# Performance work log

Hardware: AMD Instinct MI355X
Metric: run time of the kernel (lower is better)

Reference implementation:

```python
import jax, jax.numpy as jnp
import numpy as np

B, S, H, NH, HD = 2, 2048, 1024, 16, 64
RD = 16            # rotary_dim = head_dim * 0.25
W = 16             # mini_context_length (sliding window)
SCALE = HD ** -0.5
ROPE_BASE = 10000.0


def setup_inputs() -> dict:
    key = jax.random.key(0)
    ks = jax.random.split(key, 10)
    p = lambda k, shape: (jax.random.normal(k, shape, dtype=jnp.float32) * 0.02)
    return {
        "hidden_states": jax.random.normal(ks[0], (B, S, H), dtype=jnp.float32),
        "Wqkv": p(ks[1], (3 * H, H)), "bqkv": p(ks[2], (3 * H,)),
        "Wqa": p(ks[3], (H, H)),      "bqa": p(ks[4], (H,)),
        "Wka": p(ks[5], (H, H)),      "bka": p(ks[6], (H,)),
        "Wd": p(ks[7], (H, H)),       "bd": p(ks[8], (H,)),
    }


def _rotate_half(x):
    x1, x2 = jnp.split(x, 2, axis=-1)
    return jnp.concatenate([-x2, x1], axis=-1)


def _apply_rope(q, k, seq_len):
    # GPT-NeoX style rotary on the first RD dims. q,k: [B,NH,S,RD]
    inv_freq = 1.0 / (ROPE_BASE ** (jnp.arange(0, RD, 2, dtype=jnp.float32) / RD))
    t = jnp.arange(seq_len, dtype=jnp.float32)
    freqs = jnp.outer(t, inv_freq)                     # [S, RD//2]
    emb = jnp.concatenate([freqs, freqs], axis=-1)     # [S, RD]
    cos = jnp.cos(emb)[None, None]                      # [1,1,S,RD]
    sin = jnp.sin(emb)[None, None]
    return q * cos + _rotate_half(q) * sin, k * cos + _rotate_half(k) * sin


def reference(hidden_states, Wqkv, bqkv, Wqa, bqa, Wka, bka, Wd, bd):
    b, s, _ = hidden_states.shape
    qkv = hidden_states @ Wqkv.T + bqkv                       # [B,S,3H]
    qkv = qkv.reshape(b, s, 3, NH, HD).transpose(2, 0, 3, 1, 4)
    q, k, v = qkv[0], qkv[1], qkv[2]                          # [B,NH,S,HD]

    q_rot, k_rot = _apply_rope(q[..., :RD], k[..., :RD], s)
    q = jnp.concatenate([q_rot, q[..., RD:]], axis=-1)
    k = jnp.concatenate([k_rot, k[..., RD:]], axis=-1)

    # ----- Stage 1: sliding-window local attention (vectorized) -----
    pos = jnp.arange(s)
    idx = pos[:, None] - (W - 1) + jnp.arange(W)[None, :]     # [S,W]
    valid = idx >= 0
    idxc = jnp.clip(idx, 0, s - 1)
    k_win = k[:, :, idxc, :]                                   # [B,NH,S,W,HD]
    v_win = v[:, :, idxc, :]
    scores = jnp.einsum('bhsd,bhswd->bhsw', q, k_win) * SCALE
    scores = jnp.where(valid[None, None], scores, -jnp.inf)
    probs = jax.nn.softmax(scores, axis=-1)
    A = jnp.einsum('bhsw,bhswd->bhsd', probs, v_win)           # [B,NH,S,HD]

    A_hidden = A.transpose(0, 2, 1, 3).reshape(b, s, H)        # [B,S,H]

    # ----- Stage 2: causal global attention over A -----
    qa = (A_hidden @ Wqa.T + bqa).reshape(b, s, NH, HD).transpose(0, 2, 1, 3)
    ka = (A_hidden @ Wka.T + bka).reshape(b, s, NH, HD).transpose(0, 2, 1, 3)
    g = jnp.einsum('bhqd,bhkd->bhqk', qa, ka) * SCALE          # [B,NH,S,S]
    causal = pos[:, None] >= pos[None, :]
    g = jnp.where(causal[None, None], g, -jnp.inf)
    pg = jax.nn.softmax(g, axis=-1)
    out = jnp.einsum('bhqk,bhkd->bhqd', pg, A)                 # [B,NH,S,HD]
    out = out.transpose(0, 2, 1, 3).reshape(b, s, H)
    return out @ Wd.T + bd
```

## Files before the change

### kernel.cpp

```cpp
#include <hip/hip_runtime.h>
#include <hip/hip_bf16.h>
#include <cstdint>
#include <cstddef>

typedef __bf16 bf16;
typedef __bf16 bf16x4 __attribute__((ext_vector_type(4)));
typedef __bf16 bf16x8 __attribute__((ext_vector_type(8)));
typedef float  f32x4  __attribute__((ext_vector_type(4)));

#define DEVINL __device__ __forceinline__

constexpr int   Bc  = 2, Sc = 2048, Hc = 1024, NHc = 16, HDc = 64;
constexpr int   Tc  = Bc * Sc;
constexpr float L2E = 1.44269504088896340736f;
constexpr float NEG_BIG = -1.0e30f;
constexpr float INV2PI = 0.15915494309189535f;

typedef __attribute__((address_space(1))) void AS1void;
typedef __attribute__((address_space(3))) void AS3void;

DEVINL void load_lds16(const bf16* g, bf16* l) {
  __builtin_amdgcn_global_load_lds((AS1void*)g, (AS3void*)l, 16, 0, 0);
}

#if __has_builtin(__builtin_amdgcn_exp2f)
DEVINL float fast_exp2(float x) { return __builtin_amdgcn_exp2f(x); }
#else
DEVINL float fast_exp2(float x) { return exp2f(x); }
#endif

#if __has_builtin(__builtin_amdgcn_sinf) && __has_builtin(__builtin_amdgcn_cosf) && __has_builtin(__builtin_amdgcn_fractf)
DEVINL void fast_sincos_rev(float rev, float* sn, float* cs) {
  float r = __builtin_amdgcn_fractf(rev);
  *sn = __builtin_amdgcn_sinf(r);
  *cs = __builtin_amdgcn_cosf(r);
}
#else
DEVINL void fast_sincos_rev(float rev, float* sn, float* cs) {
  sincosf(rev * 6.283185307179586f, sn, cs);
}
#endif

DEVINL void xcd_remap(int& mi, int& ni) {
  const int nx  = (int)gridDim.x;
  const int nwg = nx * (int)gridDim.y;
  const int flat = (int)blockIdx.y * nx + (int)blockIdx.x;
  const int nper = nwg >> 3;
  const int neu  = (flat & 7) * nper + (flat >> 3);
  mi = neu / nx; ni = neu - mi * nx;
}

__global__ __launch_bounds__(256)
void convert_all(const float* __restrict__ hs, const float* __restrict__ Wqkv,
                 const float* __restrict__ Wqa, const float* __restrict__ Wka,
                 const float* __restrict__ Wd, const float* __restrict__ bqa,
                 const float* __restrict__ bka,
                 bf16* __restrict__ hsb, bf16* __restrict__ wqkvb,
                 bf16* __restrict__ wqakab, bf16* __restrict__ wdb,
                 float* __restrict__ bqaka) {
  const int blk = blockIdx.x;
  if (blk >= 5120) {
    const int i = threadIdx.x * 8;
    const float* src = (i < 1024) ? (bqa + i) : (bka + i - 1024);
    *(f32x4*)(bqaka + i)     = *(const f32x4*)src;
    *(f32x4*)(bqaka + i + 4) = *(const f32x4*)(src + 4);
    return;
  }
  const float* src; bf16* dst; int base;
  if      (blk < 2048) { src = hs;   dst = hsb;                    base = blk; }
  else if (blk < 3584) { src = Wqkv; dst = wqkvb;                  base = blk - 2048; }
  else if (blk < 4096) { src = Wqa;  dst = wqakab;                 base = blk - 3584; }
  else if (blk < 4608) { src = Wka;  dst = wqakab + 1024 * 1024;   base = blk - 4096; }
  else                 { src = Wd;   dst = wdb;                    base = blk - 4608; }
  const int i = (base * 256 + threadIdx.x) * 8;
  f32x4 a = *(const f32x4*)(src + i);
  f32x4 b = *(const f32x4*)(src + i + 4);
  bf16x8 v;
#pragma unroll
  for (int j = 0; j < 4; j++) { v[j] = (bf16)a[j]; v[4 + j] = (bf16)b[j]; }
  *(bf16x8*)(dst + i) = v;
}

template <typename CT>
__global__ __launch_bounds__(256, 3)
void gemm128(const bf16* __restrict__ A, const bf16* __restrict__ Bw,
             const float* __restrict__ bias, CT* __restrict__ C,
             int M, int N, int K) {
  __shared__ __attribute__((aligned(16))) bf16 As[128 * 64];
  __shared__ __attribute__((aligned(16))) bf16 Bs[128 * 64];

  const int tid = threadIdx.x, wv = tid >> 6, lane = tid & 63;
  int mi, ni; xcd_remap(mi, ni);
  const int m0 = mi * 128, n0 = ni * 128;
  const int col = lane & 15, quad = lane >> 4;
  const int wrow = (wv >> 1) * 64, wcol = (wv & 1) * 64;

  f32x4 acc[4][4];
#pragma unroll
  for (int i = 0; i < 4; i++)
#pragma unroll
    for (int j = 0; j < 4; j++) acc[i][j] = f32x4{0.f, 0.f, 0.f, 0.f};

  const int srow = tid >> 3;
  const int scol = (((tid & 7) ^ (srow & 7)) << 3);
  const bf16* Ag = A  + (size_t)(m0 + srow) * K + scol;
  const bf16* Bg = Bw + (size_t)(n0 + srow) * K + scol;
  const int cs = col & 7;

  for (int k0 = 0; k0 < K; k0 += 64) {
#pragma unroll
    for (int c = 0; c < 4; c++) {
      load_lds16(Ag + (size_t)(c * 32) * K + k0, As + c * 2048 + tid * 8);
      load_lds16(Bg + (size_t)(c * 32) * K + k0, Bs + c * 2048 + tid * 8);
    }
    __syncthreads();
#pragma unroll
    for (int kk = 0; kk < 64; kk += 32) {
      const int so = ((((kk >> 3) + quad) ^ cs) << 3);
      bf16x8 af[4], bfr[4];
#pragma unroll
      for (int i = 0; i < 4; i++)
        af[i] = *(const bf16x8*)(As + (wrow + i * 16 + col) * 64 + so);
#pragma unroll
      for (int j = 0; j < 4; j++)
        bfr[j] = *(const bf16x8*)(Bs + (wcol + j * 16 + col) * 64 + so);
#pragma unroll
      for (int i = 0; i < 4; i++)
#pragma unroll
        for (int j = 0; j < 4; j++)
          acc[i][j] = __builtin_amdgcn_mfma_f32_16x16x32_bf16(af[i], bfr[j], acc[i][j], 0, 0, 0);
    }
    __syncthreads();
  }

#pragma unroll
  for (int j = 0; j < 4; j++) {
    const int c = n0 + wcol + j * 16 + col;
    const float bv = bias[c];
#pragma unroll
    for (int i = 0; i < 4; i++)
#pragma unroll
      for (int r = 0; r < 4; r++) {
        const int rr = m0 + wrow + i * 16 + quad * 4 + r;
        C[(size_t)rr * N + c] = (CT)(acc[i][j][r] + bv);
      }
  }
}

template <typename CT>
__global__ __launch_bounds__(256, 3)
void gemm12864(const bf16* __restrict__ A, const bf16* __restrict__ Bw,
               const float* __restrict__ bias, CT* __restrict__ C,
               int M, int N, int K) {
  __shared__ __attribute__((aligned(16))) bf16 As[128 * 64];
  __shared__ __attribute__((aligned(16))) bf16 Bs[64 * 64];

  const int tid = threadIdx.x, wv = tid >> 6, lane = tid & 63;
  int mi, ni; xcd_remap(mi, ni);
  const int m0 = mi * 128, n0 = ni * 64;
  const int col = lane & 15, quad = lane >> 4;
  const int wm = wv >> 1, wn = wv & 1;

  f32x4 acc[4][2];
#pragma unroll
  for (int i = 0; i < 4; i++)
#pragma unroll
    for (int j = 0; j < 2; j++) acc[i][j] = f32x4{0.f, 0.f, 0.f, 0.f};

  const int srow = tid >> 3;
  const int scol = (((tid & 7) ^ (srow & 7)) << 3);
  const bf16* Ag = A  + (size_t)(m0 + srow) * K + scol;
  const bf16* Bg = Bw + (size_t)(n0 + srow) * K + scol;
  const int cs = col & 7;

  for (int k0 = 0; k0 < K; k0 += 64) {
#pragma unroll
    for (int c = 0; c < 4; c++)
      load_lds16(Ag + (size_t)(c * 32) * K + k0, As + c * 2048 + tid * 8);
#pragma unroll
    for (int c = 0; c < 2; c++)
      load_lds16(Bg + (size_t)(c * 32) * K + k0, Bs + c * 2048 + tid * 8);
    __syncthreads();
#pragma unroll
    for (int kk = 0; kk < 64; kk += 32) {
      const int so = ((((kk >> 3) + quad) ^ cs) << 3);
      bf16x8 af[4], bfr[2];
#pragma unroll
      for (int i = 0; i < 4; i++)
        af[i] = *(const bf16x8*)(As + (wm * 64 + i * 16 + col) * 64 + so);
#pragma unroll
      for (int j = 0; j < 2; j++)
        bfr[j] = *(const bf16x8*)(Bs + (wn * 32 + j * 16 + col) * 64 + so);
#pragma unroll
      for (int i = 0; i < 4; i++)
#pragma unroll
        for (int j = 0; j < 2; j++)
          acc[i][j] = __builtin_amdgcn_mfma_f32_16x16x32_bf16(af[i], bfr[j], acc[i][j], 0, 0, 0);
    }
    __syncthreads();
  }

#pragma unroll
  for (int j = 0; j < 2; j++) {
    const int c = n0 + wn * 32 + j * 16 + col;
    const float bv = bias[c];
#pragma unroll
    for (int i = 0; i < 4; i++)
#pragma unroll
      for (int r = 0; r < 4; r++) {
        const int rr = m0 + wm * 64 + i * 16 + quad * 4 + r;
        C[(size_t)rr * N + c] = (CT)(acc[i][j][r] + bv);
      }
  }
}

__global__ __launch_bounds__(256)
void window_attn(const bf16* __restrict__ qkv, bf16* __restrict__ Ah,
                 bf16* __restrict__ VTg) {
  __shared__ __attribute__((aligned(16))) bf16 Kw[31 * 72];
  __shared__ __attribute__((aligned(16))) bf16 Vw[31 * 72];
  const int g  = blockIdx.x;
  const int st = g & 127;
  const int h  = (g >> 7) & 15;
  const int b  = g >> 11;
  const int s0 = st * 16;
  const int tid = threadIdx.x;

  if ((tid < 124) || (tid >= 128 && tid < 252)) {
    const bool isK = tid < 124;
    const int lt  = isK ? tid : tid - 128;
    const int r   = lt >> 2, off = (lt & 3) << 4;
    int sidx = s0 - 15 + r; if (sidx < 0) sidx = 0;
    const bf16* src = qkv + (size_t)(b * Sc + sidx) * 3072 + (isK ? 1024 : 2048) + h * 64 + off;
    bf16x8 v0 = *(const bf16x8*)src;
    bf16x8 v1 = *(const bf16x8*)(src + 8);
    if (isK && off == 0) {
#pragma unroll
      for (int j = 0; j < 8; j++) {
        const float invf_rev = exp2f(-(float)j * 1.66096404744368128f) * INV2PI;
        float sn, csn;
        fast_sincos_rev((float)sidx * invf_rev, &sn, &csn);
        const float x1 = (float)v0[j], x2 = (float)v1[j];
        v0[j] = (bf16)(x1 * csn - x2 * sn);
        v1[j] = (bf16)(x2 * csn + x1 * sn);
      }
    }
    bf16* dst = (isK ? Kw : Vw) + r * 72 + off;
    *(bf16x8*)dst       = v0;
    *(bf16x8*)(dst + 8) = v1;
  }
  __syncthreads();

  const int wv = tid >> 6, lane = tid & 63;
  const int subq = lane >> 4, lane16 = lane & 15;
  const int s = s0 + wv * 4 + subq;
  const int t = b * Sc + s;
  const int d0 = lane16 * 4;

  float qd[4];
  {
    bf16x4 qv = *(const bf16x4*)(qkv + (size_t)t * 3072 + h * 64 + d0);
#pragma unroll
    for (int j = 0; j < 4; j++) qd[j] = (float)qv[j];
  }
  float pd[4];
#pragma unroll
  for (int j = 0; j < 4; j++) pd[j] = __shfl_xor(qd[j], 2, 64);
  if (lane16 < 4) {
#pragma unroll
    for (int j = 0; j < 4; j++) {
      const int jabs = d0 + j;
      const float invf_rev = exp2f(-(float)(jabs & 7) * 1.66096404744368128f) * INV2PI;
      float sn, csn;
      fast_sincos_rev((float)s * invf_rev, &sn, &csn);
      qd[j] = (jabs < 8) ? (qd[j] * csn - pd[j] * sn) : (qd[j] * csn + pd[j] * sn);
    }
  }

  float sc[16];
#pragma unroll
  for (int w = 0; w < 16; w++) {
    const int idxp = s - 15 + w;
    const int row = idxp - s0 + 15;
    bf16x4 kv = *(const bf16x4*)(Kw + row * 72 + d0);
    float p = qd[0] * (float)kv[0] + qd[1] * (float)kv[1] +
              qd[2] * (float)kv[2] + qd[3] * (float)kv[3];
#pragma unroll
    for (int m = 1; m < 16; m <<= 1) p += __shfl_xor(p, m, 64);
    sc[w] = (idxp < 0) ? NEG_BIG : p * 0.125f;
  }
  float mx = sc[0];
#pragma unroll
  for (int w = 1; w < 16; w++) mx = fmaxf(mx, sc[w]);
  float sum = 0.f;
#pragma unroll
  for (int w = 0; w < 16; w++) { sc[w] = fast_exp2((sc[w] - mx) * L2E); sum += sc[w]; }
  const float inv = 1.0f / fmaxf(sum, 1e-30f);

  float acc[4] = {0.f, 0.f, 0.f, 0.f};
#pragma unroll
  for (int w = 0; w < 16; w++) {
    const int idxp = s - 15 + w;
    const int row = idxp - s0 + 15;
    bf16x4 vv = *(const bf16x4*)(Vw + row * 72 + d0);
#pragma unroll
    for (int j = 0; j < 4; j++) acc[j] += sc[w] * (float)vv[j];
  }
  bf16x4 ov;
#pragma unroll
  for (int j = 0; j < 4; j++) ov[j] = (bf16)(acc[j] * inv);
  *(bf16x4*)(Ah + (size_t)t * 1024 + h * 64 + d0) = ov;
  bf16* vt = VTg + (((size_t)(b * 16 + h)) * 64 + d0) * 2048 + s;
#pragma unroll
  for (int j = 0; j < 4; j++) vt[(size_t)j * 2048] = ov[j];
}

__global__ __launch_bounds__(512, 2)
void flash_attn(const bf16* __restrict__ Q, const bf16* __restrict__ Kt,
                const bf16* __restrict__ VTg, bf16* __restrict__ O) {
  constexpr int QS = 2048;
  __shared__ __attribute__((aligned(16))) bf16 K_lds[3][128 * 64];
  __shared__ __attribute__((aligned(16))) bf16 VT_lds[3][64 * 128];

  const int tid = threadIdx.x, wv = tid >> 6, lane = tid & 63;
  const int bh = blockIdx.x;
  const int y  = blockIdx.y;
  const int qtA = y, qtB = 15 - y;
  const int nA = y + 1;
  const int b = bh >> 4, h = bh & 15;
  const int col = lane & 15, quad = lane >> 4;
  const size_t bS = (size_t)b * Sc;
  const int hd = h * 64;
  const int cs8 = col & 7;

  const int krow = tid >> 3;
  const int kswz = (((tid & 7) ^ (krow & 7)) << 3);
  const int vrow = tid >> 4;
  const int vswz = (((tid & 15) ^ (vrow & 15)) << 3);
  const bf16* Kg0 = Kt  + (bS * QS) + (size_t)krow * QS + hd + kswz;
  const bf16* Vg0 = VTg + ((size_t)bh * 64 + vrow) * 2048 + vswz;

  bf16x8 qA0, qA1, qB0, qB1;
  {
    constexpr float QSC = 0.125f * L2E;
    const bf16* qpA = Q + (bS + qtA * 128 + wv * 16 + col) * QS + hd + quad * 8;
    const bf16* qpB = Q + (bS + qtB * 128 + wv * 16 + col) * QS + hd + quad * 8;
    qA0 = *(const bf16x8*)qpA;
    qA1 = *(const bf16x8*)(qpA + 32);
    qB0 = *(const bf16x8*)qpB;
    qB1 = *(const bf16x8*)(qpB + 32);
#pragma unroll
    for (int j = 0; j < 8; j++) {
      qA0[j] = (bf16)((float)qA0[j] * QSC);
      qA1[j] = (bf16)((float)qA1[j] * QSC);
      qB0[j] = (bf16)((float)qB0[j] * QSC);
      qB1[j] = (bf16)((float)qB1[j] * QSC);
    }
  }

  auto stage = [&](int bufi, int k0) {
    const bf16* kg = Kg0 + (size_t)k0 * QS;
    const bf16* vg = Vg0 + k0;
#pragma unroll
    for (int c = 0; c < 2; c++) {
      load_lds16(kg + (size_t)(c * 64) * QS, K_lds[bufi] + c * 4096 + tid * 8);
      load_lds16(vg + (size_t)(c * 32) * 2048, VT_lds[bufi] + c * 4096 + tid * 8);
    }
  };
  auto k0of = [&](int i) { return ((i >= nA) ? i - nA : i) * 128; };

  f32x4 oacc[4];
#pragma unroll
  for (int i = 0; i < 4; i++) oacc[i] = f32x4{0.f, 0.f, 0.f, 0.f};
  float lsum = 0.f;

  stage(0, 0);
  stage(1, k0of(1));

  for (int it = 0; it < 17; it++) {
    const int seg  = (it >= nA);
    const int kt   = seg ? (it - nA) : it;
    const int nkt  = seg ? (17 - nA) : nA;
    const int qt   = seg ? qtB : qtA;
    const int k0   = kt * 128;
    const int qbase = qt * 128 + wv * 16;
    const int bufc = it % 3;

    if (it == 16)                      asm volatile("s_waitcnt vmcnt(0)" ::: "memory");
    else if (it == nA || it == nA + 1) asm volatile("s_waitcnt vmcnt(20)" ::: "memory");
    else                               asm volatile("s_waitcnt vmcnt(4)" ::: "memory");
    __builtin_amdgcn_s_barrier();
    __builtin_amdgcn_sched_barrier(0);

    if (it + 2 < 17) stage((it + 2) % 3, k0of(it + 2));

    bf16x8 q0, q1;
    if (seg) { q0 = qB0; q1 = qB1; } else { q0 = qA0; q1 = qA1; }

    const bf16* Kl = K_lds[bufc];
    const bf16* Vl = VT_lds[bufc];

    f32x4 sacc[8];
    __builtin_amdgcn_s_setprio(1);
#pragma unroll
    for (int sub = 0; sub < 8; sub++) {
      f32x4 a = f32x4{0.f, 0.f, 0.f, 0.f};
      {
        const int so = ((quad ^ cs8) << 3);
        bf16x8 kf = *(const bf16x8*)(Kl + (sub * 16 + col) * 64 + so);
        a = __builtin_amdgcn_mfma_f32_16x16x32_bf16(kf, q0, a, 0, 0, 0);
      }
      {
        const int so = (((4 + quad) ^ cs8) << 3);
        bf16x8 kf = *(const bf16x8*)(Kl + (sub * 16 + col) * 64 + so);
        a = __builtin_amdgcn_mfma_f32_16x16x32_bf16(kf, q1, a, 0, 0, 0);
      }
      sacc[sub] = a;
    }
    __builtin_amdgcn_s_setprio(0);

    if (kt == nkt - 1) {
      const int qq = qbase + col;
#pragma unroll
      for (int sub = 0; sub < 8; sub++)
#pragma unroll
        for (int r = 0; r < 4; r++) {
          const int key = k0 + sub * 16 + quad * 4 + r;
          if (key > qq) sacc[sub][r] = NEG_BIG;
        }
    }
#pragma unroll
    for (int sub = 0; sub < 8; sub++)
#pragma unroll
      for (int r = 0; r < 4; r++) {
        const float p = fast_exp2(sacc[sub][r]);
        sacc[sub][r] = p;
        lsum += p;
      }

#pragma unroll
    for (int t = 0; t < 4; t++) {
      uint32_t a0, a1, b0, b1;
      asm("v_cvt_pk_bf16_f32 %0, %1, %2"
          : "=v"(a0) : "v"(sacc[2 * t][0]), "v"(sacc[2 * t][1]));
      asm("v_cvt_pk_bf16_f32 %0, %1, %2"
          : "=v"(a1) : "v"(sacc[2 * t][2]), "v"(sacc[2 * t][3]));
      asm("v_cvt_pk_bf16_f32 %0, %1, %2"
          : "=v"(b0) : "v"(sacc[2 * t + 1][0]), "v"(sacc[2 * t + 1][1]));
      asm("v_cvt_pk_bf16_f32 %0, %1, %2"
          : "=v"(b1) : "v"(sacc[2 * t + 1][2]), "v"(sacc[2 * t + 1][3]));
      asm("v_permlane32_swap_b32 %0, %1" : "+v"(a0), "+v"(b0));
      asm("v_permlane16_swap_b32 %0, %1" : "+v"(a0), "+v"(b0));
      asm("v_permlane32_swap_b32 %0, %1" : "+v"(a1), "+v"(b1));
      asm("v_permlane16_swap_b32 %0, %1" : "+v"(a1), "+v"(b1));
      union { uint32_t u[4]; bf16x8 v; } pk;
      pk.u[0] = a0; pk.u[1] = a1; pk.u[2] = b0; pk.u[3] = b1;
      const int vso = (((4 * t + quad) ^ col) << 3);
      __builtin_amdgcn_s_setprio(1);
#pragma unroll
      for (int nb = 0; nb < 4; nb++) {
        bf16x8 vf = *(const bf16x8*)(Vl + (nb * 16 + col) * 128 + vso);
        oacc[nb] = __builtin_amdgcn_mfma_f32_16x16x32_bf16(pk.v, vf, oacc[nb], 0, 0, 0);
      }
      __builtin_amdgcn_s_setprio(0);
    }

    if (kt == nkt - 1) {
      float tot = lsum;
      tot += __shfl_xor(tot, 16, 64);
      tot += __shfl_xor(tot, 32, 64);
      float lrow[4];
#pragma unroll
      for (int r = 0; r < 4; r++)
        lrow[r] = 1.0f / fmaxf(__shfl(tot, quad * 4 + r, 16), 1e-37f);
#pragma unroll
      for (int nb = 0; nb < 4; nb++)
#pragma unroll
        for (int r = 0; r < 4; r++) {
          const int qq = qbase + quad * 4 + r;
          O[(bS + qq) * 1024 + hd + nb * 16 + col] = (bf16)(oacc[nb][r] * lrow[r]);
        }
#pragma unroll
      for (int i = 0; i < 4; i++) oacc[i] = f32x4{0.f, 0.f, 0.f, 0.f};
      lsum = 0.f;
    }
  }
}

extern "C" void kernel_launch(void* const* d_in, const int* in_sizes, int n_in,
                              void* d_out, int out_size, void* d_ws, size_t ws_size,
                              hipStream_t stream) {
  (void)in_sizes; (void)n_in; (void)out_size; (void)ws_size;
  const float* hs   = (const float*)d_in[0];
  const float* Wqkv = (const float*)d_in[1];
  const float* bqkv = (const float*)d_in[2];
  const float* Wqa  = (const float*)d_in[3];
  const float* bqa  = (const float*)d_in[4];
  const float* Wka  = (const float*)d_in[5];
  const float* bka  = (const float*)d_in[6];
  const float* Wd   = (const float*)d_in[7];
  const float* bd   = (const float*)d_in[8];
  float* out = (float*)d_out;

  const size_t TH = (size_t)Tc * Hc;
  bf16* dob   = (bf16*)d_out;
  bf16* hsb   = dob;
  bf16* wqkvb = dob + TH;
  bf16* Ah    = dob;
  bf16* VTg   = dob + TH;
  bf16* ws     = (bf16*)d_ws;
  bf16* qkv    = ws;
  bf16* qaka   = ws;
  bf16* oh     = ws + 2 * TH;
  bf16* wqakab = ws + 3 * TH;
  bf16* wdb    = wqakab + 2 * 1024 * 1024;
  float* bqaka = (float*)(wdb + 1024 * 1024);

  convert_all<<<dim3(5121), 256, 0, stream>>>(hs, Wqkv, Wqa, Wka, Wd, bqa, bka,
                                              hsb, wqkvb, wqakab, wdb, bqaka);

  gemm128<bf16><<<dim3(24, 32), 256, 0, stream>>>(hsb, wqkvb, bqkv, qkv, Tc, 3 * Hc, Hc);
  window_attn<<<dim3(Tc * NHc / 16), 256, 0, stream>>>(qkv, Ah, VTg);
  gemm128<bf16><<<dim3(16, 32), 256, 0, stream>>>(Ah, wqakab, bqaka, qaka, Tc, 2 * Hc, Hc);
  flash_attn<<<dim3(Bc * NHc, 8), 512, 0, stream>>>(qaka, qaka + Hc, VTg, oh);
  gemm12864<float><<<dim3(16, 32), 256, 0, stream>>>(oh, wdb, bd, out, Tc, Hc, Hc);
}
```

Baseline: 219.4 us.

## Switch flash attention to 32x32x16 MFMA with split-K warps and LDS reduction

Reworks the global causal attention kernel from 16x16x32 to 32x32x16 bf16 MFMA tiles. Waves are now split into query groups of 32 rows and two key halves per tile, and the partial outputs and row sums are merged through LDS at segment ends. Launch bounds drop to one block per SM, and the wait count is adjusted for the new load pattern. The aim is fewer MFMA instructions, fewer LDS fragment loads and fewer permlanes per tile. In exchange it adds extra barriers, LDS traffic in the epilogue, and possibly lower occupancy.

```diff
diff --git a/kernel.cpp b/kernel.cpp
--- a/kernel.cpp
+++ b/kernel.cpp
@@ -7,6 +7,7 @@
 typedef __bf16 bf16x4 __attribute__((ext_vector_type(4)));
 typedef __bf16 bf16x8 __attribute__((ext_vector_type(8)));
 typedef float  f32x4  __attribute__((ext_vector_type(4)));
+typedef float  f32x16 __attribute__((ext_vector_type(16)));
 
 #define DEVINL __device__ __forceinline__
 
@@ -40,6 +41,13 @@
   sincosf(rev * 6.283185307179586f, sn, cs);
 }
 #endif
+
+DEVINL f32x16 zero16() {
+  f32x16 z;
+#pragma unroll
+  for (int i = 0; i < 16; i++) z[i] = 0.f;
+  return z;
+}
 
 DEVINL void xcd_remap(int& mi, int& ni) {
   const int nx  = (int)gridDim.x;
@@ -315,7 +323,7 @@
   for (int j = 0; j < 4; j++) vt[(size_t)j * 2048] = ov[j];
 }
 
-__global__ __launch_bounds__(512, 2)
+__global__ __launch_bounds__(512, 1)
 void flash_attn(const bf16* __restrict__ Q, const bf16* __restrict__ Kt,
                 const bf16* __restrict__ VTg, bf16* __restrict__ O) {
   constexpr int QS = 2048;
@@ -323,15 +331,15 @@
   __shared__ __attribute__((aligned(16))) bf16 VT_lds[3][64 * 128];
 
   const int tid = threadIdx.x, wv = tid >> 6, lane = tid & 63;
+  const int qw = wv >> 1, kw = wv & 1;
   const int bh = blockIdx.x;
   const int y  = blockIdx.y;
   const int qtA = y, qtB = 15 - y;
   const int nA = y + 1;
   const int b = bh >> 4, h = bh & 15;
-  const int col = lane & 15, quad = lane >> 4;
   const size_t bS = (size_t)b * Sc;
   const int hd = h * 64;
-  const int cs8 = col & 7;
+  const int l31 = lane & 31, lhi = lane >> 5, l15 = lane & 15, l7 = lane & 7;
 
   const int krow = tid >> 3;
   const int kswz = (((tid & 7) ^ (krow & 7)) << 3);
@@ -340,21 +348,21 @@
   const bf16* Kg0 = Kt  + (bS * QS) + (size_t)krow * QS + hd + kswz;
   const bf16* Vg0 = VTg + ((size_t)bh * 64 + vrow) * 2048 + vswz;
 
-  bf16x8 qA0, qA1, qB0, qB1;
+  bf16x8 qA0, qA1, qA2, qA3, qB0, qB1, qB2, qB3;
   {
     constexpr float QSC = 0.125f * L2E;
-    const bf16* qpA = Q + (bS + qtA * 128 + wv * 16 + col) * QS + hd + quad * 8;
-    const bf16* qpB = Q + (bS + qtB * 128 + wv * 16 + col) * QS + hd + quad * 8;
-    qA0 = *(const bf16x8*)qpA;
-    qA1 = *(const bf16x8*)(qpA + 32);
-    qB0 = *(const bf16x8*)qpB;
-    qB1 = *(const bf16x8*)(qpB + 32);
+    const bf16* pA = Q + (bS + qtA * 128 + qw * 32 + l31) * QS + hd + lhi * 8;
+    const bf16* pB = Q + (bS + qtB * 128 + qw * 32 + l31) * QS + hd + lhi * 8;
+    qA0 = *(const bf16x8*)(pA);      qA1 = *(const bf16x8*)(pA + 16);
+    qA2 = *(const bf16x8*)(pA + 32); qA3 = *(const bf16x8*)(pA + 48);
+    qB0 = *(const bf16x8*)(pB);      qB1 = *(const bf16x8*)(pB + 16);
+    qB2 = *(const bf16x8*)(pB + 32); qB3 = *(const bf16x8*)(pB + 48);
 #pragma unroll
     for (int j = 0; j < 8; j++) {
-      qA0[j] = (bf16)((float)qA0[j] * QSC);
-      qA1[j] = (bf16)((float)qA1[j] * QSC);
-      qB0[j] = (bf16)((float)qB0[j] * QSC);
-      qB1[j] = (bf16)((float)qB1[j] * QSC);
+      qA0[j] = (bf16)((float)qA0[j] * QSC); qA1[j] = (bf16)((float)qA1[j] * QSC);
+      qA2[j] = (bf16)((float)qA2[j] * QSC); qA3[j] = (bf16)((float)qA3[j] * QSC);
+      qB0[j] = (bf16)((float)qB0[j] * QSC); qB1[j] = (bf16)((float)qB1[j] * QSC);
+      qB2[j] = (bf16)((float)qB2[j] * QSC); qB3[j] = (bf16)((float)qB3[j] * QSC);
     }
   }
 
@@ -369,9 +377,7 @@
   };
   auto k0of = [&](int i) { return ((i >= nA) ? i - nA : i) * 128; };
 
-  f32x4 oacc[4];
-#pragma unroll
-  for (int i = 0; i < 4; i++) oacc[i] = f32x4{0.f, 0.f, 0.f, 0.f};
+  f32x16 oacc0 = zero16(), oacc1 = zero16();
   float lsum = 0.f;
 
   stage(0, 0);
@@ -383,105 +389,142 @@
     const int nkt  = seg ? (17 - nA) : nA;
     const int qt   = seg ? qtB : qtA;
     const int k0   = kt * 128;
-    const int qbase = qt * 128 + wv * 16;
+    const int qbase = qt * 128 + qw * 32;
     const int bufc = it % 3;
 
     if (it == 16)                      asm volatile("s_waitcnt vmcnt(0)" ::: "memory");
-    else if (it == nA || it == nA + 1) asm volatile("s_waitcnt vmcnt(20)" ::: "memory");
+    else if (it == nA || it == nA + 1) asm volatile("s_waitcnt vmcnt(8)" ::: "memory");
     else                               asm volatile("s_waitcnt vmcnt(4)" ::: "memory");
     __builtin_amdgcn_s_barrier();
     __builtin_amdgcn_sched_barrier(0);
 
     if (it + 2 < 17) stage((it + 2) % 3, k0of(it + 2));
 
-    bf16x8 q0, q1;
-    if (seg) { q0 = qB0; q1 = qB1; } else { q0 = qA0; q1 = qA1; }
+    bf16x8 q0, q1, q2, q3;
+    if (seg) { q0 = qB0; q1 = qB1; q2 = qB2; q3 = qB3; }
+    else     { q0 = qA0; q1 = qA1; q2 = qA2; q3 = qA3; }
 
     const bf16* Kl = K_lds[bufc];
     const bf16* Vl = VT_lds[bufc];
 
-    f32x4 sacc[8];
+    f32x16 s0_ = zero16(), s1_ = zero16();
     __builtin_amdgcn_s_setprio(1);
-#pragma unroll
-    for (int sub = 0; sub < 8; sub++) {
-      f32x4 a = f32x4{0.f, 0.f, 0.f, 0.f};
-      {
-        const int so = ((quad ^ cs8) << 3);
-        bf16x8 kf = *(const bf16x8*)(Kl + (sub * 16 + col) * 64 + so);
-        a = __builtin_amdgcn_mfma_f32_16x16x32_bf16(kf, q0, a, 0, 0, 0);
-      }
-      {
-        const int so = (((4 + quad) ^ cs8) << 3);
-        bf16x8 kf = *(const bf16x8*)(Kl + (sub * 16 + col) * 64 + so);
-        a = __builtin_amdgcn_mfma_f32_16x16x32_bf16(kf, q1, a, 0, 0, 0);
-      }
-      sacc[sub] = a;
+    {
+      const int kr0 = ((kw * 2 + 0) * 32 + l31) * 64;
+      const int kr1 = ((kw * 2 + 1) * 32 + l31) * 64;
+#pragma unroll
+      for (int dc = 0; dc < 4; dc++) {
+        const int so = (((2 * dc + lhi) ^ l7) << 3);
+        bf16x8 qf = (dc == 0) ? q0 : (dc == 1) ? q1 : (dc == 2) ? q2 : q3;
+        bf16x8 kf0 = *(const bf16x8*)(Kl + kr0 + so);
+        s0_ = __builtin_amdgcn_mfma_f32_32x32x16_bf16(kf0, qf, s0_, 0, 0, 0);
+        bf16x8 kf1 = *(const bf16x8*)(Kl + kr1 + so);
+        s1_ = __builtin_amdgcn_mfma_f32_32x32x16_bf16(kf1, qf, s1_, 0, 0, 0);
+      }
     }
     __builtin_amdgcn_s_setprio(0);
 
     if (kt == nkt - 1) {
-      const int qq = qbase + col;
-#pragma unroll
-      for (int sub = 0; sub < 8; sub++)
-#pragma unroll
-        for (int r = 0; r < 4; r++) {
-          const int key = k0 + sub * 16 + quad * 4 + r;
-          if (key > qq) sacc[sub][r] = NEG_BIG;
+      const int qq = qbase + l31;
+      const int kb0 = k0 + kw * 64;
+#pragma unroll
+      for (int r = 0; r < 16; r++) {
+        const int ky = kb0 + (r & 3) + 8 * (r >> 2) + 4 * lhi;
+        if (ky > qq)      s0_[r] = NEG_BIG;
+        if (ky + 32 > qq) s1_[r] = NEG_BIG;
+      }
+    }
+#pragma unroll
+    for (int r = 0; r < 16; r++) {
+      const float p0 = fast_exp2(s0_[r]); s0_[r] = p0; lsum += p0;
+      const float p1 = fast_exp2(s1_[r]); s1_[r] = p1; lsum += p1;
+    }
+
+#define PV_STEP(SACC, KB, F)                                                   \
+    {                                                                          \
+      uint32_t a0, a1, b0, b1;                                                 \
+      asm("v_cvt_pk_bf16_f32 %0, %1, %2" : "=v"(a0)                            \
+          : "v"(SACC[(F)*8 + 0]), "v"(SACC[(F)*8 + 1]));                       \
+      asm("v_cvt_pk_bf16_f32 %0, %1, %2" : "=v"(a1)                            \
+          : "v"(SACC[(F)*8 + 2]), "v"(SACC[(F)*8 + 3]));                       \
+      asm("v_cvt_pk_bf16_f32 %0, %1, %2" : "=v"(b0)                            \
+          : "v"(SACC[(F)*8 + 4]), "v"(SACC[(F)*8 + 5]));                       \
+      asm("v_cvt_pk_bf16_f32 %0, %1, %2" : "=v"(b1)                            \
+          : "v"(SACC[(F)*8 + 6]), "v"(SACC[(F)*8 + 7]));                       \
+      asm("v_permlane32_swap_b32 %0, %1" : "+v"(a0), "+v"(b0));                \
+      asm("v_permlane32_swap_b32 %0, %1" : "+v"(a1), "+v"(b1));                \
+      union { uint32_t u[4]; bf16x8 v; } pk;                                   \
+      pk.u[0] = a0; pk.u[1] = a1; pk.u[2] = b0; pk.u[3] = b1;                  \
+      const int kc = kw * 8 + (KB) * 4 + (F) * 2;                              \
+      const int vso = (((kc + lhi) ^ l15) << 3);                               \
+      __builtin_amdgcn_s_setprio(1);                                           \
+      { bf16x8 vf = *(const bf16x8*)(Vl + (l31) * 128 + vso);                  \
+        oacc0 = __builtin_amdgcn_mfma_f32_32x32x16_bf16(vf, pk.v, oacc0, 0, 0, 0); } \
+      { bf16x8 vf = *(const bf16x8*)(Vl + (32 + l31) * 128 + vso);             \
+        oacc1 = __builtin_amdgcn_mfma_f32_32x32x16_bf16(vf, pk.v, oacc1, 0, 0, 0); } \
+      __builtin_amdgcn_s_setprio(0);                                           \
+    }
+    PV_STEP(s0_, 0, 0)
+    PV_STEP(s0_, 0, 1)
+    PV_STEP(s1_, 1, 0)
+    PV_STEP(s1_, 1, 1)
+#undef PV_STEP
+
+    if (kt == nkt - 1) {
+      float totw = lsum + __shfl_xor(lsum, 32, 64);
+      asm volatile("s_waitcnt lgkmcnt(0)" ::: "memory");
+      __builtin_amdgcn_s_barrier();
+      float* Kf = (float*)(&K_lds[bufc][0]);
+      float* Vf = (float*)(&VT_lds[bufc][0]);
+      float* slot = Kf + qw * 1024 + (lane << 4);
+      if (lhi == 0) Vf[kw * 128 + qw * 32 + l31] = totw;
+      if (kw == 1) {
+#pragma unroll
+        for (int g = 0; g < 4; g++)
+          *(f32x4*)(slot + 4 * g) = f32x4{oacc0[4 * g], oacc0[4 * g + 1],
+                                          oacc0[4 * g + 2], oacc0[4 * g + 3]};
+      }
+      asm volatile("s_waitcnt lgkmcnt(0)" ::: "memory");
+      __builtin_amdgcn_s_barrier();
+      __builtin_amdgcn_sched_barrier(0);
+      const int q = qbase + l31;
+      bf16* Op = O + (bS + q) * 1024 + hd + kw * 32 + 4 * lhi;
+      const float ptot = Vf[(kw ^ 1) * 128 + qw * 32 + l31];
+      const float inv = 1.0f / fmaxf(totw + ptot, 1e-37f);
+      if (kw == 0) {
+#pragma unroll
+        for (int g = 0; g < 4; g++) {
+          f32x4 po = *(const f32x4*)(slot + 4 * g);
+          bf16x4 ov;
+#pragma unroll
+          for (int j = 0; j < 4; j++)
+            ov[j] = (bf16)((oacc0[4 * g + j] + po[j]) * inv);
+          *(bf16x4*)(Op + 8 * g) = ov;
         }
-    }
-#pragma unroll
-    for (int sub = 0; sub < 8; sub++)
-#pragma unroll
-      for (int r = 0; r < 4; r++) {
-        const float p = fast_exp2(sacc[sub][r]);
-        sacc[sub][r] = p;
-        lsum += p;
-      }
-
-#pragma unroll
-    for (int t = 0; t < 4; t++) {
-      uint32_t a0, a1, b0, b1;
-      asm("v_cvt_pk_bf16_f32 %0, %1, %2"
-          : "=v"(a0) : "v"(sacc[2 * t][0]), "v"(sacc[2 * t][1]));
-      asm("v_cvt_pk_bf16_f32 %0, %1, %2"
-          : "=v"(a1) : "v"(sacc[2 * t][2]), "v"(sacc[2 * t][3]));
-      asm("v_cvt_pk_bf16_f32 %0, %1, %2"
-          : "=v"(b0) : "v"(sacc[2 * t + 1][0]), "v"(sacc[2 * t + 1][1]));
-      asm("v_cvt_pk_bf16_f32 %0, %1, %2"
-          : "=v"(b1) : "v"(sacc[2 * t + 1][2]), "v"(sacc[2 * t + 1][3]));
-      asm("v_permlane32_swap_b32 %0, %1" : "+v"(a0), "+v"(b0));
-      asm("v_permlane16_swap_b32 %0, %1" : "+v"(a0), "+v"(b0));
-      asm("v_permlane32_swap_b32 %0, %1" : "+v"(a1), "+v"(b1));
-      asm("v_permlane16_swap_b32 %0, %1" : "+v"(a1), "+v"(b1));
-      union { uint32_t u[4]; bf16x8 v; } pk;
-      pk.u[0] = a0; pk.u[1] = a1; pk.u[2] = b0; pk.u[3] = b1;
-      const int vso = (((4 * t + quad) ^ col) << 3);
-      __builtin_amdgcn_s_setprio(1);
-#pragma unroll
-      for (int nb = 0; nb < 4; nb++) {
-        bf16x8 vf = *(const bf16x8*)(Vl + (nb * 16 + col) * 128 + vso);
-        oacc[nb] = __builtin_amdgcn_mfma_f32_16x16x32_bf16(pk.v, vf, oacc[nb], 0, 0, 0);
-      }
-      __builtin_amdgcn_s_setprio(0);
-    }
-
-    if (kt == nkt - 1) {
-      float tot = lsum;
-      tot += __shfl_xor(tot, 16, 64);
-      tot += __shfl_xor(tot, 32, 64);
-      float lrow[4];
-#pragma unroll
-      for (int r = 0; r < 4; r++)
-        lrow[r] = 1.0f / fmaxf(__shfl(tot, quad * 4 + r, 16), 1e-37f);
-#pragma unroll
-      for (int nb = 0; nb < 4; nb++)
-#pragma unroll
-        for (int r = 0; r < 4; r++) {
-          const int qq = qbase + quad * 4 + r;
-          O[(bS + qq) * 1024 + hd + nb * 16 + col] = (bf16)(oacc[nb][r] * lrow[r]);
+      }
+      asm volatile("s_waitcnt lgkmcnt(0)" ::: "memory");
+      __builtin_amdgcn_s_barrier();
+      if (kw == 0) {
+#pragma unroll
+        for (int g = 0; g < 4; g++)
+          *(f32x4*)(slot + 4 * g) = f32x4{oacc1[4 * g], oacc1[4 * g + 1],
+                                          oacc1[4 * g + 2], oacc1[4 * g + 3]};
+      }
+      asm volatile("s_waitcnt lgkmcnt(0)" ::: "memory");
+      __builtin_amdgcn_s_barrier();
+      __builtin_amdgcn_sched_barrier(0);
+      if (kw == 1) {
+#pragma unroll
+        for (int g = 0; g < 4; g++) {
+          f32x4 po = *(const f32x4*)(slot + 4 * g);
+          bf16x4 ov;
+#pragma unroll
+          for (int j = 0; j < 4; j++)
+            ov[j] = (bf16)((oacc1[4 * g + j] + po[j]) * inv);
+          *(bf16x4*)(Op + 8 * g) = ov;
         }
-#pragma unroll
-      for (int i = 0; i < 4; i++) oacc[i] = f32x4{0.f, 0.f, 0.f, 0.f};
+      }
+      oacc0 = zero16(); oacc1 = zero16();
       lsum = 0.f;
     }
   }
```

New measurement: 218.3 us, median of 2. No clear change (-0.5%).
